# Kernel optimization log

Measured on AMD Instinct MI355X. Metric: run time of the kernel, lower is better.

Reference implementation:

```python
import jax, jax.numpy as jnp
import numpy as np

MARGIN = 0.3
BIG = 1e6  # matches the 1000000.0 additive mask in the torch code


def setup_inputs() -> dict:
    key = jax.random.key(0)
    k1, k2 = jax.random.split(key)
    embeddings = jax.random.normal(k1, (4096, 512), dtype=jnp.float32)
    labels = jax.random.randint(k2, (4096,), 0, 512)
    return {"embeddings": embeddings, "labels": labels}


def reference(embeddings, labels):
    # Pairwise euclidean distances (torch.cdist p=2) via the GEMM identity,
    # clamped before sqrt for numerical safety on the zero diagonal.
    sq = jnp.sum(embeddings * embeddings, axis=1)                      # [N]
    d2 = sq[:, None] + sq[None, :] - 2.0 * (embeddings @ embeddings.T)  # [N, N]
    dist = jnp.sqrt(jnp.maximum(d2, 1e-12))

    pos_mask = labels[None, :] == labels[:, None]   # [N, N] bool
    neg_mask = ~pos_mask

    # Hardest positive per anchor (self-distance 0 is harmless under max).
    hp = jnp.max(dist * pos_mask.astype(dist.dtype), axis=1)           # [N]

    # Semi-hard negatives: hp < d(a, n) < hp + margin, different label.
    semi_hard = (dist > hp[:, None]) & (dist < hp[:, None] + MARGIN) & neg_mask
    has_semi_hard = jnp.sum(semi_hard) > 0

    # Fallback: hardest (farthest) negative; semi-hard branch: closest semi-hard.
    hn_fallback = jnp.max(dist * neg_mask.astype(dist.dtype), axis=1)
    hn_semi = jnp.min(dist + (1.0 - semi_hard.astype(dist.dtype)) * BIG, axis=1)
    hn = jnp.where(has_semi_hard, hn_semi, hn_fallback)                # [N]

    triplet = jax.nn.relu(hp - hn + MARGIN)                            # [N]
    num_valid = jnp.sum((triplet > 0).astype(triplet.dtype))
    loss = jnp.where(num_valid > 0,
                     jnp.sum(triplet) / jnp.maximum(num_valid, 1.0),
                     jnp.mean(triplet))
    return loss
```

## Files before the change

kernel.cpp:

```cpp
#include <hip/hip_runtime.h>
#include <math.h>


constexpr float MARGIN = 0.3f;

typedef _Float16 half8    __attribute__((ext_vector_type(8)));
typedef float    floatx16 __attribute__((ext_vector_type(16)));

#define GLD_LDS16(gp, lp)                                                              \
    __builtin_amdgcn_global_load_lds(                                                  \
        (const __attribute__((address_space(1))) void*)(gp),                           \
        (__attribute__((address_space(3))) void*)(lp), 16, 0, 0)

__global__ __launch_bounds__(256)
void prep_kernel(const float* __restrict__ e, _Float16* __restrict__ pan,
                 float* __restrict__ sq, unsigned int* __restrict__ hp,
                 unsigned int* __restrict__ hn_fall, unsigned int* __restrict__ hn_semi,
                 unsigned int* __restrict__ bars, int N, int D) {
    if (blockIdx.x == 0 && threadIdx.x < 32) bars[threadIdx.x * 32] = 0u;
    const int r0  = blockIdx.x * 32;
    const int p   = r0 >> 7;
    const int rl  = r0 & 127;
    const int r   = threadIdx.x >> 3;
    const int c8  = threadIdx.x & 7;
    const int row = r0 + r;
    const float* er = e + (size_t)row * D;
    float s = 0.f;
    #pragma unroll
    for (int it = 0; it < 8; ++it) {
        const int kw = c8 + it * 8;
        const float4 x0 = *(const float4*)&er[kw * 8];
        const float4 x1 = *(const float4*)&er[kw * 8 + 4];
        const float xv[8] = {x0.x, x0.y, x0.z, x0.w, x1.x, x1.y, x1.z, x1.w};
        half8 hi, lo;
        #pragma unroll
        for (int j = 0; j < 8; ++j) {
            _Float16 h = (_Float16)xv[j];
            hi[j] = h;
            lo[j] = (_Float16)(xv[j] - (float)h);
            s += xv[j] * xv[j];
        }
        *(half8*)&pan[((size_t)(p * 128 + kw) * 128 + rl + r) * 8]      = hi;
        *(half8*)&pan[((size_t)(p * 128 + 64 + kw) * 128 + rl + r) * 8] = lo;
    }
    s += __shfl_down(s, 4, 8);
    s += __shfl_down(s, 2, 8);
    s += __shfl_down(s, 1, 8);
    if (c8 == 0) {
        sq[row]      = s;
        hp[row]      = 0u;
        hn_fall[row] = 0u;
        hn_semi[row] = 0x7f800000u;
    }
}

__global__ __launch_bounds__(512, 4)
void fused_kernel(const _Float16* __restrict__ pan, const int* __restrict__ labels,
                  const float* __restrict__ sq,
                  unsigned int* __restrict__ hp,
                  unsigned int* __restrict__ hn_fall,
                  unsigned int* __restrict__ hn_semi,
                  unsigned int* __restrict__ bars,
                  float* __restrict__ out,
                  int N, int D, unsigned int nrowblocks, unsigned int nblocks) {
    __shared__ __attribute__((aligned(16))) _Float16 S[2][12288];
    __shared__ float sq_r[256], sq_c[128], hp_r[256];
    __shared__ int   lab_r[256], lab_c[128];
    __shared__ int   lastflag;

    const int tid  = threadIdx.x;
    const int lane = tid & 63;
    const int wave = tid >> 6;
    const int wr = (wave >> 1) * 64;
    const int wc = (wave & 1) * 64;
    const int mrow = lane & 31;
    const int half_id = lane >> 5;

    const int j  = blockIdx.x & 7;
    const int i  = blockIdx.x >> 3;
    const int px = (j & 3) * 8 + (i & 7);
    const int py = (j >> 2) * 8 + (i >> 3);
    const int rowBase = py * 256;
    const int colBase = px * 128;

    if (tid < 256) {
        sq_r[tid]  = sq[rowBase + tid];
        lab_r[tid] = labels[rowBase + tid];
    } else if (tid < 384) {
        const int t = tid - 256;
        sq_c[t]  = sq[colBase + t];
        lab_c[t] = labels[colBase + t];
    }

    floatx16 acc[2][2];
    #pragma unroll
    for (int a = 0; a < 2; ++a)
        #pragma unroll
        for (int b = 0; b < 2; ++b)
            #pragma unroll
            for (int r = 0; r < 16; ++r) acc[a][b][r] = 0.f;

    auto stage = [&](int b, int kkv) {
        #pragma unroll
        for (int t = 0; t < 3; ++t) {
            const int s = wave * 3 + t;
            int kcl, p, row0, lofs;
            if (s < 16) {
                const int rq = s & 3;
                kcl  = s >> 2;
                p    = 2 * py + (rq >> 1);
                row0 = (rq & 1) * 64;
                lofs = (kcl * 256 + rq * 64) * 8;
            } else {
                const int u = s - 16;
                kcl  = u >> 1;
                p    = px;
                row0 = (u & 1) * 64;
                lofs = 8192 + (kcl * 128 + row0) * 8;
            }
            const int kc = (kcl < 2) ? (2 * kkv + kcl) : (64 + 2 * kkv + (kcl - 2));
            const _Float16* g = pan + ((size_t)(p * 128 + kc) * 128 + row0 + lane) * 8;
            GLD_LDS16(g, &S[b][lofs]);
        }
    };

    stage(0, 0);

    #pragma unroll 1
    for (int kk = 0; kk < 32; ++kk) {
        const int b = kk & 1;
        __syncthreads();
        if (kk + 1 < 32) stage(b ^ 1, kk + 1);
        const int rA = wr + mrow, cB = wc + mrow;
        const half8 ah0 = *(const half8*)&S[b][(half_id * 256 + rA) * 8];
        const half8 ah1 = *(const half8*)&S[b][(half_id * 256 + rA + 32) * 8];
        const half8 al0 = *(const half8*)&S[b][((2 + half_id) * 256 + rA) * 8];
        const half8 al1 = *(const half8*)&S[b][((2 + half_id) * 256 + rA + 32) * 8];
        const half8 bh0 = *(const half8*)&S[b][8192 + (half_id * 128 + cB) * 8];
        const half8 bh1 = *(const half8*)&S[b][8192 + (half_id * 128 + cB + 32) * 8];
        const half8 bl0 = *(const half8*)&S[b][8192 + ((2 + half_id) * 128 + cB) * 8];
        const half8 bl1 = *(const half8*)&S[b][8192 + ((2 + half_id) * 128 + cB + 32) * 8];
        acc[0][0] = __builtin_amdgcn_mfma_f32_32x32x16_f16(bh0, ah0, acc[0][0], 0, 0, 0);
        acc[0][1] = __builtin_amdgcn_mfma_f32_32x32x16_f16(bh0, ah1, acc[0][1], 0, 0, 0);
        acc[1][0] = __builtin_amdgcn_mfma_f32_32x32x16_f16(bh1, ah0, acc[1][0], 0, 0, 0);
        acc[1][1] = __builtin_amdgcn_mfma_f32_32x32x16_f16(bh1, ah1, acc[1][1], 0, 0, 0);
        acc[0][0] = __builtin_amdgcn_mfma_f32_32x32x16_f16(bl0, ah0, acc[0][0], 0, 0, 0);
        acc[0][1] = __builtin_amdgcn_mfma_f32_32x32x16_f16(bl0, ah1, acc[0][1], 0, 0, 0);
        acc[1][0] = __builtin_amdgcn_mfma_f32_32x32x16_f16(bl1, ah0, acc[1][0], 0, 0, 0);
        acc[1][1] = __builtin_amdgcn_mfma_f32_32x32x16_f16(bl1, ah1, acc[1][1], 0, 0, 0);
        acc[0][0] = __builtin_amdgcn_mfma_f32_32x32x16_f16(bh0, al0, acc[0][0], 0, 0, 0);
        acc[0][1] = __builtin_amdgcn_mfma_f32_32x32x16_f16(bh0, al1, acc[0][1], 0, 0, 0);
        acc[1][0] = __builtin_amdgcn_mfma_f32_32x32x16_f16(bh1, al0, acc[1][0], 0, 0, 0);
        acc[1][1] = __builtin_amdgcn_mfma_f32_32x32x16_f16(bh1, al1, acc[1][1], 0, 0, 0);
    }

    float sqr[2]; int labr[2];
    #pragma unroll
    for (int ai = 0; ai < 2; ++ai) {
        sqr[ai]  = sq_r[wr + ai * 32 + mrow];
        labr[ai] = lab_r[wr + ai * 32 + mrow];
    }

    #pragma unroll
    for (int ai = 0; ai < 2; ++ai) {
        float vp = 0.f, vn = 0.f;
        #pragma unroll
        for (int bj = 0; bj < 2; ++bj) {
            #pragma unroll
            for (int r = 0; r < 16; ++r) {
                const int c = wc + bj * 32 + (r & 3) + 8 * (r >> 2) + 4 * half_id;
                float d = sqrtf(fmaxf(sqr[ai] + sq_c[c] - 2.0f * acc[bj][ai][r], 1e-12f));
                const bool pos = (labr[ai] == lab_c[c]);
                vp = fmaxf(vp, pos ? d : 0.f);
                vn = fmaxf(vn, pos ? 0.f : d);
            }
        }
        vp = fmaxf(vp, __shfl_xor(vp, 32, 64));
        vn = fmaxf(vn, __shfl_xor(vn, 32, 64));
        if (half_id == 0) {
            atomicMax(&hp[rowBase + wr + ai * 32 + mrow],      __float_as_uint(vp));
            atomicMax(&hn_fall[rowBase + wr + ai * 32 + mrow], __float_as_uint(vn));
        }
    }

    __syncthreads();
    unsigned int* ctr = &bars[py * 32];
    if (tid == 0) {
        __threadfence();
        atomicAdd(ctr, 1u);
        while (__hip_atomic_load(ctr, __ATOMIC_ACQUIRE, __HIP_MEMORY_SCOPE_AGENT)
               < nrowblocks)
            __builtin_amdgcn_s_sleep(32);
    }
    __syncthreads();
    if (tid < 256)
        hp_r[tid] = __uint_as_float(__hip_atomic_load(&hp[rowBase + tid],
                                    __ATOMIC_RELAXED, __HIP_MEMORY_SCOPE_AGENT));
    __syncthreads();

    #pragma unroll
    for (int ai = 0; ai < 2; ++ai) {
        const float hpv = hp_r[wr + ai * 32 + mrow];
        float vm = __builtin_inff();
        #pragma unroll
        for (int bj = 0; bj < 2; ++bj) {
            #pragma unroll
            for (int r = 0; r < 16; ++r) {
                const int c = wc + bj * 32 + (r & 3) + 8 * (r >> 2) + 4 * half_id;
                float d = sqrtf(fmaxf(sqr[ai] + sq_c[c] - 2.0f * acc[bj][ai][r], 1e-12f));
                const bool cand = (labr[ai] != lab_c[c]) && (d > hpv);
                vm = fminf(vm, cand ? d : __builtin_inff());
            }
        }
        vm = fminf(vm, __shfl_xor(vm, 32, 64));
        if (half_id == 0)
            atomicMin(&hn_semi[rowBase + wr + ai * 32 + mrow], __float_as_uint(vm));
    }

    __syncthreads();
    if (tid == 0) {
        __threadfence();
        unsigned int old = atomicAdd(&bars[992], 1u);
        lastflag = (old == nblocks - 1) ? 1 : 0;
    }
    __syncthreads();
    if (!lastflag) return;
    if (tid == 0) __threadfence();
    __syncthreads();

    float* FS = (float*)&S[0][0];
    int*   IC = (int*)(FS + 512);
    int*   IA = IC + 512;
    int any = 0;
    for (int r = tid; r < N; r += 512) {
        float h  = __uint_as_float(__hip_atomic_load(&hp[r],      __ATOMIC_RELAXED, __HIP_MEMORY_SCOPE_AGENT));
        float hs = __uint_as_float(__hip_atomic_load(&hn_semi[r], __ATOMIC_RELAXED, __HIP_MEMORY_SCOPE_AGENT));
        any |= (hs < h + MARGIN) ? 1 : 0;
    }
    IA[tid] = any;
    __syncthreads();
    for (int s = 256; s; s >>= 1) {
        if (tid < s) IA[tid] |= IA[tid + s];
        __syncthreads();
    }
    const bool has_semi = IA[0] != 0;
    float sum = 0.f; int valid = 0;
    for (int r = tid; r < N; r += 512) {
        float h  = __uint_as_float(__hip_atomic_load(&hp[r], __ATOMIC_RELAXED, __HIP_MEMORY_SCOPE_AGENT));
        float hn = has_semi
            ? __uint_as_float(__hip_atomic_load(&hn_semi[r], __ATOMIC_RELAXED, __HIP_MEMORY_SCOPE_AGENT))
            : __uint_as_float(__hip_atomic_load(&hn_fall[r], __ATOMIC_RELAXED, __HIP_MEMORY_SCOPE_AGENT));
        float t = fmaxf(h - hn + MARGIN, 0.f);
        if (!(t > 0.f)) t = 0.f;
        sum += t;
        valid += (t > 0.f) ? 1 : 0;
    }
    FS[tid] = sum; IC[tid] = valid;
    __syncthreads();
    for (int s = 256; s; s >>= 1) {
        if (tid < s) { FS[tid] += FS[tid + s]; IC[tid] += IC[tid + s]; }
        __syncthreads();
    }
    if (tid == 0) {
        float total = FS[0]; int v = IC[0];
        out[0] = (v > 0) ? (total / (float)v) : (total / (float)N);
    }
}

extern "C" void kernel_launch(void* const* d_in, const int* in_sizes, int n_in,
                              void* d_out, int out_size, void* d_ws, size_t ws_size,
                              hipStream_t stream) {
    const float* e      = (const float*)d_in[0];
    const int*   labels = (const int*)d_in[1];
    const int N = in_sizes[1];
    const int D = in_sizes[0] / N;
    float* out = (float*)d_out;

    float*        sq      = (float*)d_ws;
    unsigned int* hp      = (unsigned int*)d_ws + N;
    unsigned int* hn_fall = hp + N;
    unsigned int* hn_semi = hn_fall + N;
    unsigned int* bars    = hn_semi + N;

    const size_t small_bytes = ((size_t)(4 * N + 1024) * 4 + 255) & ~(size_t)255;
    _Float16* pan = (_Float16*)((char*)d_ws + small_bytes);

    prep_kernel<<<N / 32, 256, 0, stream>>>(e, pan, sq, hp, hn_fall, hn_semi, bars, N, D);

    const int ntx = N / 128, nty = N / 256;
    fused_kernel<<<ntx * nty, 512, 0, stream>>>(pan, labels, sq, hp, hn_fall, hn_semi,
                                                bars, out, N, D,
                                                (unsigned)ntx, (unsigned)(ntx * nty));
}
```

Before: 139.1 us.

## Exploit distance symmetry: compute only upper-triangle tiles with column-side reductions

Changes the fused kernel to launch only upper-triangular 128x128 tiles of the symmetric distance matrix. Each off-diagonal tile reduces both rows and columns, writing the column maxima and minima through an LDS transpose buffer. The per-row barrier now waits on both the row and the column tile counters. This roughly halves the GEMM and epilogue work, at the cost of extra LDS reductions, more atomics and a more complex spin barrier that requires all blocks to be co-resident. The prep kernel is also re-split to 16 rows per block.

```diff
diff --git a/kernel.cpp b/kernel.cpp
--- a/kernel.cpp
+++ b/kernel.cpp
@@ -17,18 +17,21 @@
                  float* __restrict__ sq, unsigned int* __restrict__ hp,
                  unsigned int* __restrict__ hn_fall, unsigned int* __restrict__ hn_semi,
                  unsigned int* __restrict__ bars, int N, int D) {
-    if (blockIdx.x == 0 && threadIdx.x < 32) bars[threadIdx.x * 32] = 0u;
-    const int r0  = blockIdx.x * 32;
+    if (blockIdx.x == 0) {
+        if (threadIdx.x < 32) bars[threadIdx.x * 32] = 0u;
+        if (threadIdx.x == 32) bars[1023] = 0u;
+    }
+    const int r0  = blockIdx.x * 16;
     const int p   = r0 >> 7;
     const int rl  = r0 & 127;
-    const int r   = threadIdx.x >> 3;
-    const int c8  = threadIdx.x & 7;
+    const int r   = threadIdx.x >> 4;
+    const int c16 = threadIdx.x & 15;
     const int row = r0 + r;
     const float* er = e + (size_t)row * D;
     float s = 0.f;
     #pragma unroll
-    for (int it = 0; it < 8; ++it) {
-        const int kw = c8 + it * 8;
+    for (int it = 0; it < 4; ++it) {
+        const int kw = c16 + it * 16;
         const float4 x0 = *(const float4*)&er[kw * 8];
         const float4 x1 = *(const float4*)&er[kw * 8 + 4];
         const float xv[8] = {x0.x, x0.y, x0.z, x0.w, x1.x, x1.y, x1.z, x1.w};
@@ -43,10 +46,11 @@
         *(half8*)&pan[((size_t)(p * 128 + kw) * 128 + rl + r) * 8]      = hi;
         *(half8*)&pan[((size_t)(p * 128 + 64 + kw) * 128 + rl + r) * 8] = lo;
     }
-    s += __shfl_down(s, 4, 8);
-    s += __shfl_down(s, 2, 8);
-    s += __shfl_down(s, 1, 8);
-    if (c8 == 0) {
+    s += __shfl_down(s, 8, 16);
+    s += __shfl_down(s, 4, 16);
+    s += __shfl_down(s, 2, 16);
+    s += __shfl_down(s, 1, 16);
+    if (c16 == 0) {
         sq[row]      = s;
         hp[row]      = 0u;
         hn_fall[row] = 0u;
@@ -54,7 +58,7 @@
     }
 }
 
-__global__ __launch_bounds__(512, 4)
+__global__ __launch_bounds__(256, 4)
 void fused_kernel(const _Float16* __restrict__ pan, const int* __restrict__ labels,
                   const float* __restrict__ sq,
                   unsigned int* __restrict__ hp,
@@ -62,11 +66,13 @@
                   unsigned int* __restrict__ hn_semi,
                   unsigned int* __restrict__ bars,
                   float* __restrict__ out,
-                  int N, int D, unsigned int nrowblocks, unsigned int nblocks) {
-    __shared__ __attribute__((aligned(16))) _Float16 S[2][12288];
-    __shared__ float sq_r[256], sq_c[128], hp_r[256];
-    __shared__ int   lab_r[256], lab_c[128];
+                  int N, int D, int nt, unsigned int nblocks) {
+    __shared__ __attribute__((aligned(16))) unsigned char SMEM[33024];
+    __shared__ float sq_r[128], sq_c[128], hp_r[128], hp_c[128];
+    __shared__ int   lab_r[128], lab_c[128];
     __shared__ int   lastflag;
+    _Float16* S      = (_Float16*)SMEM;
+    float*    colbuf = (float*)SMEM;
 
     const int tid  = threadIdx.x;
     const int lane = tid & 63;
@@ -76,18 +82,17 @@
     const int mrow = lane & 31;
     const int half_id = lane >> 5;
 
-    const int j  = blockIdx.x & 7;
-    const int i  = blockIdx.x >> 3;
-    const int px = (j & 3) * 8 + (i & 7);
-    const int py = (j >> 2) * 8 + (i >> 3);
-    const int rowBase = py * 256;
-    const int colBase = px * 128;
-
-    if (tid < 256) {
+    int py = 0, rem = blockIdx.x;
+    while (rem >= nt - py) { rem -= nt - py; ++py; }
+    const int px = py + rem;
+    const bool diag = (px == py);
+    const int rowBase = py * 128, colBase = px * 128;
+
+    if (tid < 128) {
         sq_r[tid]  = sq[rowBase + tid];
         lab_r[tid] = labels[rowBase + tid];
-    } else if (tid < 384) {
-        const int t = tid - 256;
+    } else {
+        const int t = tid - 128;
         sq_c[t]  = sq[colBase + t];
         lab_c[t] = labels[colBase + t];
     }
@@ -102,44 +107,34 @@
 
     auto stage = [&](int b, int kkv) {
         #pragma unroll
-        for (int t = 0; t < 3; ++t) {
-            const int s = wave * 3 + t;
-            int kcl, p, row0, lofs;
-            if (s < 16) {
-                const int rq = s & 3;
-                kcl  = s >> 2;
-                p    = 2 * py + (rq >> 1);
-                row0 = (rq & 1) * 64;
-                lofs = (kcl * 256 + rq * 64) * 8;
-            } else {
-                const int u = s - 16;
-                kcl  = u >> 1;
-                p    = px;
-                row0 = (u & 1) * 64;
-                lofs = 8192 + (kcl * 128 + row0) * 8;
-            }
+        for (int t = 0; t < 4; ++t) {
+            const int slab = wave * 4 + t;
+            const int side = slab >> 3;
+            const int u = slab & 7;
+            const int kcl = u >> 1, rh = u & 1;
+            const int pp = side ? px : py;
             const int kc = (kcl < 2) ? (2 * kkv + kcl) : (64 + 2 * kkv + (kcl - 2));
-            const _Float16* g = pan + ((size_t)(p * 128 + kc) * 128 + row0 + lane) * 8;
-            GLD_LDS16(g, &S[b][lofs]);
+            const _Float16* g = pan + ((size_t)(pp * 128 + kc) * 128 + rh * 64 + lane) * 8;
+            GLD_LDS16(g, &S[b * 8192 + side * 4096 + (kcl * 128 + rh * 64) * 8]);
         }
     };
 
     stage(0, 0);
-
     #pragma unroll 1
     for (int kk = 0; kk < 32; ++kk) {
         const int b = kk & 1;
         __syncthreads();
         if (kk + 1 < 32) stage(b ^ 1, kk + 1);
+        const _Float16* Sb = S + b * 8192;
         const int rA = wr + mrow, cB = wc + mrow;
-        const half8 ah0 = *(const half8*)&S[b][(half_id * 256 + rA) * 8];
-        const half8 ah1 = *(const half8*)&S[b][(half_id * 256 + rA + 32) * 8];
-        const half8 al0 = *(const half8*)&S[b][((2 + half_id) * 256 + rA) * 8];
-        const half8 al1 = *(const half8*)&S[b][((2 + half_id) * 256 + rA + 32) * 8];
-        const half8 bh0 = *(const half8*)&S[b][8192 + (half_id * 128 + cB) * 8];
-        const half8 bh1 = *(const half8*)&S[b][8192 + (half_id * 128 + cB + 32) * 8];
-        const half8 bl0 = *(const half8*)&S[b][8192 + ((2 + half_id) * 128 + cB) * 8];
-        const half8 bl1 = *(const half8*)&S[b][8192 + ((2 + half_id) * 128 + cB + 32) * 8];
+        const half8 ah0 = *(const half8*)&Sb[(half_id * 128 + rA) * 8];
+        const half8 ah1 = *(const half8*)&Sb[(half_id * 128 + rA + 32) * 8];
+        const half8 al0 = *(const half8*)&Sb[((2 + half_id) * 128 + rA) * 8];
+        const half8 al1 = *(const half8*)&Sb[((2 + half_id) * 128 + rA + 32) * 8];
+        const half8 bh0 = *(const half8*)&Sb[4096 + (half_id * 128 + cB) * 8];
+        const half8 bh1 = *(const half8*)&Sb[4096 + (half_id * 128 + cB + 32) * 8];
+        const half8 bl0 = *(const half8*)&Sb[4096 + ((2 + half_id) * 128 + cB) * 8];
+        const half8 bl1 = *(const half8*)&Sb[4096 + ((2 + half_id) * 128 + cB + 32) * 8];
         acc[0][0] = __builtin_amdgcn_mfma_f32_32x32x16_f16(bh0, ah0, acc[0][0], 0, 0, 0);
         acc[0][1] = __builtin_amdgcn_mfma_f32_32x32x16_f16(bh0, ah1, acc[0][1], 0, 0, 0);
         acc[1][0] = __builtin_amdgcn_mfma_f32_32x32x16_f16(bh1, ah0, acc[1][0], 0, 0, 0);
@@ -153,6 +148,7 @@
         acc[1][0] = __builtin_amdgcn_mfma_f32_32x32x16_f16(bh1, al0, acc[1][0], 0, 0, 0);
         acc[1][1] = __builtin_amdgcn_mfma_f32_32x32x16_f16(bh1, al1, acc[1][1], 0, 0, 0);
     }
+    __syncthreads();
 
     float sqr[2]; int labr[2];
     #pragma unroll
@@ -160,21 +156,23 @@
         sqr[ai]  = sq_r[wr + ai * 32 + mrow];
         labr[ai] = lab_r[wr + ai * 32 + mrow];
     }
+    auto distf = [&](int bj, int ai, int r, int c) {
+        return sqrtf(fmaxf(sqr[ai] + sq_c[c] - 2.0f * acc[bj][ai][r], 1e-12f));
+    };
 
     #pragma unroll
     for (int ai = 0; ai < 2; ++ai) {
         float vp = 0.f, vn = 0.f;
         #pragma unroll
-        for (int bj = 0; bj < 2; ++bj) {
+        for (int bj = 0; bj < 2; ++bj)
             #pragma unroll
             for (int r = 0; r < 16; ++r) {
                 const int c = wc + bj * 32 + (r & 3) + 8 * (r >> 2) + 4 * half_id;
-                float d = sqrtf(fmaxf(sqr[ai] + sq_c[c] - 2.0f * acc[bj][ai][r], 1e-12f));
+                const float d = distf(bj, ai, r, c);
                 const bool pos = (labr[ai] == lab_c[c]);
                 vp = fmaxf(vp, pos ? d : 0.f);
                 vn = fmaxf(vn, pos ? 0.f : d);
             }
-        }
         vp = fmaxf(vp, __shfl_xor(vp, 32, 64));
         vn = fmaxf(vn, __shfl_xor(vn, 32, 64));
         if (half_id == 0) {
@@ -183,19 +181,54 @@
         }
     }
 
-    __syncthreads();
-    unsigned int* ctr = &bars[py * 32];
+    const int rr = (wave >> 1) * 32 + mrow;
+    if (!diag) {
+        #pragma unroll
+        for (int kind = 0; kind < 2; ++kind) {
+            #pragma unroll
+            for (int bj = 0; bj < 2; ++bj)
+                #pragma unroll
+                for (int r = 0; r < 16; ++r) {
+                    const int c = wc + bj * 32 + (r & 3) + 8 * (r >> 2) + 4 * half_id;
+                    const float d0 = distf(bj, 0, r, c);
+                    const float d1 = distf(bj, 1, r, c);
+                    const bool p0 = (labr[0] == lab_c[c]), p1 = (labr[1] == lab_c[c]);
+                    float v;
+                    if (kind == 0) v = fmaxf(p0 ? d0 : 0.f, p1 ? d1 : 0.f);
+                    else           v = fmaxf(p0 ? 0.f : d0, p1 ? 0.f : d1);
+                    colbuf[rr * 129 + c] = v;
+                }
+            __syncthreads();
+            if (tid < 128) {
+                float v = 0.f;
+                #pragma unroll 4
+                for (int q = 0; q < 64; ++q) v = fmaxf(v, colbuf[q * 129 + tid]);
+                if (kind == 0) atomicMax(&hp[colBase + tid],      __float_as_uint(v));
+                else           atomicMax(&hn_fall[colBase + tid], __float_as_uint(v));
+            }
+            __syncthreads();
+        }
+    }
+
+    __syncthreads();
     if (tid == 0) {
         __threadfence();
-        atomicAdd(ctr, 1u);
-        while (__hip_atomic_load(ctr, __ATOMIC_ACQUIRE, __HIP_MEMORY_SCOPE_AGENT)
-               < nrowblocks)
-            __builtin_amdgcn_s_sleep(32);
-    }
-    __syncthreads();
-    if (tid < 256)
+        atomicAdd(&bars[py * 32], 1u);
+        if (!diag) atomicAdd(&bars[px * 32], 1u);
+        while (__hip_atomic_load(&bars[py * 32], __ATOMIC_ACQUIRE, __HIP_MEMORY_SCOPE_AGENT)
+               < (unsigned)nt) __builtin_amdgcn_s_sleep(32);
+        while (__hip_atomic_load(&bars[px * 32], __ATOMIC_ACQUIRE, __HIP_MEMORY_SCOPE_AGENT)
+               < (unsigned)nt) __builtin_amdgcn_s_sleep(32);
+    }
+    __syncthreads();
+    if (tid < 128)
         hp_r[tid] = __uint_as_float(__hip_atomic_load(&hp[rowBase + tid],
                                     __ATOMIC_RELAXED, __HIP_MEMORY_SCOPE_AGENT));
+    else {
+        const int t = tid - 128;
+        hp_c[t] = __uint_as_float(__hip_atomic_load(&hp[colBase + t],
+                                  __ATOMIC_RELAXED, __HIP_MEMORY_SCOPE_AGENT));
+    }
     __syncthreads();
 
     #pragma unroll
@@ -203,24 +236,46 @@
         const float hpv = hp_r[wr + ai * 32 + mrow];
         float vm = __builtin_inff();
         #pragma unroll
-        for (int bj = 0; bj < 2; ++bj) {
+        for (int bj = 0; bj < 2; ++bj)
             #pragma unroll
             for (int r = 0; r < 16; ++r) {
                 const int c = wc + bj * 32 + (r & 3) + 8 * (r >> 2) + 4 * half_id;
-                float d = sqrtf(fmaxf(sqr[ai] + sq_c[c] - 2.0f * acc[bj][ai][r], 1e-12f));
+                const float d = distf(bj, ai, r, c);
                 const bool cand = (labr[ai] != lab_c[c]) && (d > hpv);
                 vm = fminf(vm, cand ? d : __builtin_inff());
             }
-        }
         vm = fminf(vm, __shfl_xor(vm, 32, 64));
         if (half_id == 0)
             atomicMin(&hn_semi[rowBase + wr + ai * 32 + mrow], __float_as_uint(vm));
     }
 
+    if (!diag) {
+        #pragma unroll
+        for (int bj = 0; bj < 2; ++bj)
+            #pragma unroll
+            for (int r = 0; r < 16; ++r) {
+                const int c = wc + bj * 32 + (r & 3) + 8 * (r >> 2) + 4 * half_id;
+                const float hpv = hp_c[c];
+                const float d0 = distf(bj, 0, r, c);
+                const float d1 = distf(bj, 1, r, c);
+                const bool c0 = (labr[0] != lab_c[c]) && (d0 > hpv);
+                const bool c1 = (labr[1] != lab_c[c]) && (d1 > hpv);
+                colbuf[rr * 129 + c] = fminf(c0 ? d0 : __builtin_inff(),
+                                             c1 ? d1 : __builtin_inff());
+            }
+        __syncthreads();
+        if (tid < 128) {
+            float v = __builtin_inff();
+            #pragma unroll 4
+            for (int q = 0; q < 64; ++q) v = fminf(v, colbuf[q * 129 + tid]);
+            atomicMin(&hn_semi[colBase + tid], __float_as_uint(v));
+        }
+    }
+
     __syncthreads();
     if (tid == 0) {
         __threadfence();
-        unsigned int old = atomicAdd(&bars[992], 1u);
+        unsigned int old = atomicAdd(&bars[1023], 1u);
         lastflag = (old == nblocks - 1) ? 1 : 0;
     }
     __syncthreads();
@@ -228,24 +283,24 @@
     if (tid == 0) __threadfence();
     __syncthreads();
 
-    float* FS = (float*)&S[0][0];
-    int*   IC = (int*)(FS + 512);
-    int*   IA = IC + 512;
+    float* FS = (float*)SMEM;
+    int*   IC = (int*)(FS + 256);
+    int*   IA = IC + 256;
     int any = 0;
-    for (int r = tid; r < N; r += 512) {
+    for (int r = tid; r < N; r += 256) {
         float h  = __uint_as_float(__hip_atomic_load(&hp[r],      __ATOMIC_RELAXED, __HIP_MEMORY_SCOPE_AGENT));
         float hs = __uint_as_float(__hip_atomic_load(&hn_semi[r], __ATOMIC_RELAXED, __HIP_MEMORY_SCOPE_AGENT));
         any |= (hs < h + MARGIN) ? 1 : 0;
     }
     IA[tid] = any;
     __syncthreads();
-    for (int s = 256; s; s >>= 1) {
+    for (int s = 128; s; s >>= 1) {
         if (tid < s) IA[tid] |= IA[tid + s];
         __syncthreads();
     }
     const bool has_semi = IA[0] != 0;
     float sum = 0.f; int valid = 0;
-    for (int r = tid; r < N; r += 512) {
+    for (int r = tid; r < N; r += 256) {
         float h  = __uint_as_float(__hip_atomic_load(&hp[r], __ATOMIC_RELAXED, __HIP_MEMORY_SCOPE_AGENT));
         float hn = has_semi
             ? __uint_as_float(__hip_atomic_load(&hn_semi[r], __ATOMIC_RELAXED, __HIP_MEMORY_SCOPE_AGENT))
@@ -257,7 +312,7 @@
     }
     FS[tid] = sum; IC[tid] = valid;
     __syncthreads();
-    for (int s = 256; s; s >>= 1) {
+    for (int s = 128; s; s >>= 1) {
         if (tid < s) { FS[tid] += FS[tid + s]; IC[tid] += IC[tid + s]; }
         __syncthreads();
     }
@@ -285,10 +340,10 @@
     const size_t small_bytes = ((size_t)(4 * N + 1024) * 4 + 255) & ~(size_t)255;
     _Float16* pan = (_Float16*)((char*)d_ws + small_bytes);
 
-    prep_kernel<<<N / 32, 256, 0, stream>>>(e, pan, sq, hp, hn_fall, hn_semi, bars, N, D);
-
-    const int ntx = N / 128, nty = N / 256;
-    fused_kernel<<<ntx * nty, 512, 0, stream>>>(pan, labels, sq, hp, hn_fall, hn_semi,
-                                                bars, out, N, D,
-                                                (unsigned)ntx, (unsigned)(ntx * nty));
+    prep_kernel<<<N / 16, 256, 0, stream>>>(e, pan, sq, hp, hn_fall, hn_semi, bars, N, D);
+
+    const int nt = N / 128;
+    const int nblocks = nt * (nt + 1) / 2;
+    fused_kernel<<<nblocks, 256, 0, stream>>>(pan, labels, sq, hp, hn_fall, hn_semi,
+                                              bars, out, N, D, nt, (unsigned)nblocks);
 }
```

Result: slower. 151.6 us (+9.0%).

## Convert fp32 to split fp16 inside GEMM loop and defer sqrt to finalize

Applied to the files above, without the earlier changes.

Drops the separate prepacked fp16 hi/lo panel buffer. The fused kernel now loads fp32 embeddings into registers, splits them into hi/lo halves and writes them to LDS, with register prefetch of the next k-slice. It also keeps squared distances through the max/min reductions and applies sqrt only in the final reduction, removing per-element sqrt from the epilogue. This trades the panel write and read round trip for redundant conversion work in every tile and ordinary global loads in place of the direct global-to-LDS loads.

```diff
diff --git a/kernel.cpp b/kernel.cpp
--- a/kernel.cpp
+++ b/kernel.cpp
@@ -7,59 +7,39 @@
 typedef _Float16 half8    __attribute__((ext_vector_type(8)));
 typedef float    floatx16 __attribute__((ext_vector_type(16)));
 
-#define GLD_LDS16(gp, lp)                                                              \
-    __builtin_amdgcn_global_load_lds(                                                  \
-        (const __attribute__((address_space(1))) void*)(gp),                           \
-        (__attribute__((address_space(3))) void*)(lp), 16, 0, 0)
-
 __global__ __launch_bounds__(256)
-void prep_kernel(const float* __restrict__ e, _Float16* __restrict__ pan,
-                 float* __restrict__ sq, unsigned int* __restrict__ hp,
-                 unsigned int* __restrict__ hn_fall, unsigned int* __restrict__ hn_semi,
-                 unsigned int* __restrict__ bars, int N, int D) {
+void sq_init_kernel(const float* __restrict__ e, float* __restrict__ sq,
+                    unsigned int* __restrict__ hp2, unsigned int* __restrict__ hnf2,
+                    unsigned int* __restrict__ hns2, unsigned int* __restrict__ bars,
+                    int N, int D) {
     if (blockIdx.x == 0 && threadIdx.x < 32) bars[threadIdx.x * 32] = 0u;
-    const int r0  = blockIdx.x * 32;
-    const int p   = r0 >> 7;
-    const int rl  = r0 & 127;
-    const int r   = threadIdx.x >> 3;
-    const int c8  = threadIdx.x & 7;
-    const int row = r0 + r;
+    const int row  = blockIdx.x * 4 + (threadIdx.x >> 6);
+    const int lane = threadIdx.x & 63;
+    if (row >= N) return;
     const float* er = e + (size_t)row * D;
     float s = 0.f;
-    #pragma unroll
-    for (int it = 0; it < 8; ++it) {
-        const int kw = c8 + it * 8;
-        const float4 x0 = *(const float4*)&er[kw * 8];
-        const float4 x1 = *(const float4*)&er[kw * 8 + 4];
-        const float xv[8] = {x0.x, x0.y, x0.z, x0.w, x1.x, x1.y, x1.z, x1.w};
-        half8 hi, lo;
-        #pragma unroll
-        for (int j = 0; j < 8; ++j) {
-            _Float16 h = (_Float16)xv[j];
-            hi[j] = h;
-            lo[j] = (_Float16)(xv[j] - (float)h);
-            s += xv[j] * xv[j];
-        }
-        *(half8*)&pan[((size_t)(p * 128 + kw) * 128 + rl + r) * 8]      = hi;
-        *(half8*)&pan[((size_t)(p * 128 + 64 + kw) * 128 + rl + r) * 8] = lo;
-    }
-    s += __shfl_down(s, 4, 8);
-    s += __shfl_down(s, 2, 8);
-    s += __shfl_down(s, 1, 8);
-    if (c8 == 0) {
-        sq[row]      = s;
-        hp[row]      = 0u;
-        hn_fall[row] = 0u;
-        hn_semi[row] = 0x7f800000u;
+    for (int k0 = lane * 8; k0 < D; k0 += 512) {
+        const float4 x0 = *(const float4*)&er[k0];
+        const float4 x1 = *(const float4*)&er[k0 + 4];
+        s += x0.x*x0.x + x0.y*x0.y + x0.z*x0.z + x0.w*x0.w
+           + x1.x*x1.x + x1.y*x1.y + x1.z*x1.z + x1.w*x1.w;
+    }
+    #pragma unroll
+    for (int off = 32; off; off >>= 1) s += __shfl_down(s, off, 64);
+    if (lane == 0) {
+        sq[row]   = s;
+        hp2[row]  = 0u;
+        hnf2[row] = 0u;
+        hns2[row] = 0x7f800000u;
     }
 }
 
 __global__ __launch_bounds__(512, 4)
-void fused_kernel(const _Float16* __restrict__ pan, const int* __restrict__ labels,
+void fused_kernel(const float* __restrict__ e, const int* __restrict__ labels,
                   const float* __restrict__ sq,
-                  unsigned int* __restrict__ hp,
-                  unsigned int* __restrict__ hn_fall,
-                  unsigned int* __restrict__ hn_semi,
+                  unsigned int* __restrict__ hp2,
+                  unsigned int* __restrict__ hnf2,
+                  unsigned int* __restrict__ hns2,
                   unsigned int* __restrict__ bars,
                   float* __restrict__ out,
                   int N, int D, unsigned int nrowblocks, unsigned int nblocks) {
@@ -100,37 +80,53 @@
             #pragma unroll
             for (int r = 0; r < 16; ++r) acc[a][b][r] = 0.f;
 
-    auto stage = [&](int b, int kkv) {
-        #pragma unroll
-        for (int t = 0; t < 3; ++t) {
-            const int s = wave * 3 + t;
-            int kcl, p, row0, lofs;
-            if (s < 16) {
-                const int rq = s & 3;
-                kcl  = s >> 2;
-                p    = 2 * py + (rq >> 1);
-                row0 = (rq & 1) * 64;
-                lofs = (kcl * 256 + rq * 64) * 8;
-            } else {
-                const int u = s - 16;
-                kcl  = u >> 1;
-                p    = px;
-                row0 = (u & 1) * 64;
-                lofs = 8192 + (kcl * 128 + row0) * 8;
-            }
-            const int kc = (kcl < 2) ? (2 * kkv + kcl) : (64 + 2 * kkv + (kcl - 2));
-            const _Float16* g = pan + ((size_t)(p * 128 + kc) * 128 + row0 + lane) * 8;
-            GLD_LDS16(g, &S[b][lofs]);
+    const int srow = tid >> 1, sch = tid & 1;
+    float4 ra0, ra1, rb0, rb1;
+    auto loadRegs = [&](int kkv) {
+        const float* ga = &e[(size_t)(rowBase + srow) * D + kkv * 16 + sch * 8];
+        ra0 = *(const float4*)ga;
+        ra1 = *(const float4*)(ga + 4);
+        if (tid < 256) {
+            const float* gb = &e[(size_t)(colBase + srow) * D + kkv * 16 + sch * 8];
+            rb0 = *(const float4*)gb;
+            rb1 = *(const float4*)(gb + 4);
         }
     };
-
-    stage(0, 0);
+    auto cvtWrite = [&](int b) {
+        {
+            const float xv[8] = {ra0.x, ra0.y, ra0.z, ra0.w, ra1.x, ra1.y, ra1.z, ra1.w};
+            half8 hi, lo;
+            #pragma unroll
+            for (int q = 0; q < 8; ++q) {
+                _Float16 h = (_Float16)xv[q];
+                hi[q] = h;
+                lo[q] = (_Float16)(xv[q] - (float)h);
+            }
+            *(half8*)&S[b][(sch * 256 + srow) * 8]       = hi;
+            *(half8*)&S[b][((2 + sch) * 256 + srow) * 8] = lo;
+        }
+        if (tid < 256) {
+            const float xv[8] = {rb0.x, rb0.y, rb0.z, rb0.w, rb1.x, rb1.y, rb1.z, rb1.w};
+            half8 hi, lo;
+            #pragma unroll
+            for (int q = 0; q < 8; ++q) {
+                _Float16 h = (_Float16)xv[q];
+                hi[q] = h;
+                lo[q] = (_Float16)(xv[q] - (float)h);
+            }
+            *(half8*)&S[b][8192 + (sch * 128 + srow) * 8]       = hi;
+            *(half8*)&S[b][8192 + ((2 + sch) * 128 + srow) * 8] = lo;
+        }
+    };
+
+    loadRegs(0);
 
     #pragma unroll 1
     for (int kk = 0; kk < 32; ++kk) {
         const int b = kk & 1;
+        cvtWrite(b);
         __syncthreads();
-        if (kk + 1 < 32) stage(b ^ 1, kk + 1);
+        if (kk + 1 < 32) loadRegs(kk + 1);
         const int rA = wr + mrow, cB = wc + mrow;
         const half8 ah0 = *(const half8*)&S[b][(half_id * 256 + rA) * 8];
         const half8 ah1 = *(const half8*)&S[b][(half_id * 256 + rA + 32) * 8];
@@ -169,17 +165,17 @@
             #pragma unroll
             for (int r = 0; r < 16; ++r) {
                 const int c = wc + bj * 32 + (r & 3) + 8 * (r >> 2) + 4 * half_id;
-                float d = sqrtf(fmaxf(sqr[ai] + sq_c[c] - 2.0f * acc[bj][ai][r], 1e-12f));
+                const float d2 = fmaxf(sqr[ai] + sq_c[c] - 2.0f * acc[bj][ai][r], 1e-12f);
                 const bool pos = (labr[ai] == lab_c[c]);
-                vp = fmaxf(vp, pos ? d : 0.f);
-                vn = fmaxf(vn, pos ? 0.f : d);
+                vp = fmaxf(vp, pos ? d2 : 0.f);
+                vn = fmaxf(vn, pos ? 0.f : d2);
             }
         }
         vp = fmaxf(vp, __shfl_xor(vp, 32, 64));
         vn = fmaxf(vn, __shfl_xor(vn, 32, 64));
         if (half_id == 0) {
-            atomicMax(&hp[rowBase + wr + ai * 32 + mrow],      __float_as_uint(vp));
-            atomicMax(&hn_fall[rowBase + wr + ai * 32 + mrow], __float_as_uint(vn));
+            atomicMax(&hp2[rowBase + wr + ai * 32 + mrow],  __float_as_uint(vp));
+            atomicMax(&hnf2[rowBase + wr + ai * 32 + mrow], __float_as_uint(vn));
         }
     }
 
@@ -194,27 +190,27 @@
     }
     __syncthreads();
     if (tid < 256)
-        hp_r[tid] = __uint_as_float(__hip_atomic_load(&hp[rowBase + tid],
+        hp_r[tid] = __uint_as_float(__hip_atomic_load(&hp2[rowBase + tid],
                                     __ATOMIC_RELAXED, __HIP_MEMORY_SCOPE_AGENT));
     __syncthreads();
 
     #pragma unroll
     for (int ai = 0; ai < 2; ++ai) {
-        const float hpv = hp_r[wr + ai * 32 + mrow];
+        const float hpv2 = hp_r[wr + ai * 32 + mrow];
         float vm = __builtin_inff();
         #pragma unroll
         for (int bj = 0; bj < 2; ++bj) {
             #pragma unroll
             for (int r = 0; r < 16; ++r) {
                 const int c = wc + bj * 32 + (r & 3) + 8 * (r >> 2) + 4 * half_id;
-                float d = sqrtf(fmaxf(sqr[ai] + sq_c[c] - 2.0f * acc[bj][ai][r], 1e-12f));
-                const bool cand = (labr[ai] != lab_c[c]) && (d > hpv);
-                vm = fminf(vm, cand ? d : __builtin_inff());
+                const float d2 = fmaxf(sqr[ai] + sq_c[c] - 2.0f * acc[bj][ai][r], 1e-12f);
+                const bool cand = (labr[ai] != lab_c[c]) && (d2 > hpv2);
+                vm = fminf(vm, cand ? d2 : __builtin_inff());
             }
         }
         vm = fminf(vm, __shfl_xor(vm, 32, 64));
         if (half_id == 0)
-            atomicMin(&hn_semi[rowBase + wr + ai * 32 + mrow], __float_as_uint(vm));
+            atomicMin(&hns2[rowBase + wr + ai * 32 + mrow], __float_as_uint(vm));
     }
 
     __syncthreads();
@@ -233,8 +229,8 @@
     int*   IA = IC + 512;
     int any = 0;
     for (int r = tid; r < N; r += 512) {
-        float h  = __uint_as_float(__hip_atomic_load(&hp[r],      __ATOMIC_RELAXED, __HIP_MEMORY_SCOPE_AGENT));
-        float hs = __uint_as_float(__hip_atomic_load(&hn_semi[r], __ATOMIC_RELAXED, __HIP_MEMORY_SCOPE_AGENT));
+        float h  = sqrtf(__uint_as_float(__hip_atomic_load(&hp2[r],  __ATOMIC_RELAXED, __HIP_MEMORY_SCOPE_AGENT)));
+        float hs = sqrtf(__uint_as_float(__hip_atomic_load(&hns2[r], __ATOMIC_RELAXED, __HIP_MEMORY_SCOPE_AGENT)));
         any |= (hs < h + MARGIN) ? 1 : 0;
     }
     IA[tid] = any;
@@ -246,10 +242,10 @@
     const bool has_semi = IA[0] != 0;
     float sum = 0.f; int valid = 0;
     for (int r = tid; r < N; r += 512) {
-        float h  = __uint_as_float(__hip_atomic_load(&hp[r], __ATOMIC_RELAXED, __HIP_MEMORY_SCOPE_AGENT));
+        float h  = sqrtf(__uint_as_float(__hip_atomic_load(&hp2[r], __ATOMIC_RELAXED, __HIP_MEMORY_SCOPE_AGENT)));
         float hn = has_semi
-            ? __uint_as_float(__hip_atomic_load(&hn_semi[r], __ATOMIC_RELAXED, __HIP_MEMORY_SCOPE_AGENT))
-            : __uint_as_float(__hip_atomic_load(&hn_fall[r], __ATOMIC_RELAXED, __HIP_MEMORY_SCOPE_AGENT));
+            ? sqrtf(__uint_as_float(__hip_atomic_load(&hns2[r], __ATOMIC_RELAXED, __HIP_MEMORY_SCOPE_AGENT)))
+            : sqrtf(__uint_as_float(__hip_atomic_load(&hnf2[r], __ATOMIC_RELAXED, __HIP_MEMORY_SCOPE_AGENT)));
         float t = fmaxf(h - hn + MARGIN, 0.f);
         if (!(t > 0.f)) t = 0.f;
         sum += t;
@@ -276,19 +272,16 @@
     const int D = in_sizes[0] / N;
     float* out = (float*)d_out;
 
-    float*        sq      = (float*)d_ws;
-    unsigned int* hp      = (unsigned int*)d_ws + N;
-    unsigned int* hn_fall = hp + N;
-    unsigned int* hn_semi = hn_fall + N;
-    unsigned int* bars    = hn_semi + N;
-
-    const size_t small_bytes = ((size_t)(4 * N + 1024) * 4 + 255) & ~(size_t)255;
-    _Float16* pan = (_Float16*)((char*)d_ws + small_bytes);
-
-    prep_kernel<<<N / 32, 256, 0, stream>>>(e, pan, sq, hp, hn_fall, hn_semi, bars, N, D);
+    float*        sq   = (float*)d_ws;
+    unsigned int* hp2  = (unsigned int*)d_ws + N;
+    unsigned int* hnf2 = hp2 + N;
+    unsigned int* hns2 = hnf2 + N;
+    unsigned int* bars = hns2 + N;
+
+    sq_init_kernel<<<N / 4, 256, 0, stream>>>(e, sq, hp2, hnf2, hns2, bars, N, D);
 
     const int ntx = N / 128, nty = N / 256;
-    fused_kernel<<<ntx * nty, 512, 0, stream>>>(pan, labels, sq, hp, hn_fall, hn_semi,
+    fused_kernel<<<ntx * nty, 512, 0, stream>>>(e, labels, sq, hp2, hnf2, hns2,
                                                 bars, out, N, D,
                                                 (unsigned)ntx, (unsigned)(ntx * nty));
 }
```

New measurement: 146.4 us. +5.3%, slower.

## Load A operand fragments directly from global memory, stage only B in LDS

Applied to the files above, without the earlier changes.

The A-tile (row) fragments are now read straight from global memory into registers each k-step instead of going through the shared-memory double buffer. Only the B (column) tile is still staged in LDS, which shrinks the shared buffer from 48KB to 16KB and removes A's LDS write/read traffic. Each pair of waves sharing rows now fetches the same A data from global/L2 separately. The global loads issue before the barrier with no explicit prefetch, so their latency may sit on the critical path.

```diff
diff --git a/kernel.cpp b/kernel.cpp
--- a/kernel.cpp
+++ b/kernel.cpp
@@ -63,7 +63,7 @@
                   unsigned int* __restrict__ bars,
                   float* __restrict__ out,
                   int N, int D, unsigned int nrowblocks, unsigned int nblocks) {
-    __shared__ __attribute__((aligned(16))) _Float16 S[2][12288];
+    __shared__ __attribute__((aligned(16))) _Float16 S[2][4096];
     __shared__ float sq_r[256], sq_c[128], hp_r[256];
     __shared__ int   lab_r[256], lab_c[128];
     __shared__ int   lastflag;
@@ -100,46 +100,34 @@
             #pragma unroll
             for (int r = 0; r < 16; ++r) acc[a][b][r] = 0.f;
 
-    auto stage = [&](int b, int kkv) {
-        #pragma unroll
-        for (int t = 0; t < 3; ++t) {
-            const int s = wave * 3 + t;
-            int kcl, p, row0, lofs;
-            if (s < 16) {
-                const int rq = s & 3;
-                kcl  = s >> 2;
-                p    = 2 * py + (rq >> 1);
-                row0 = (rq & 1) * 64;
-                lofs = (kcl * 256 + rq * 64) * 8;
-            } else {
-                const int u = s - 16;
-                kcl  = u >> 1;
-                p    = px;
-                row0 = (u & 1) * 64;
-                lofs = 8192 + (kcl * 128 + row0) * 8;
-            }
-            const int kc = (kcl < 2) ? (2 * kkv + kcl) : (64 + 2 * kkv + (kcl - 2));
-            const _Float16* g = pan + ((size_t)(p * 128 + kc) * 128 + row0 + lane) * 8;
-            GLD_LDS16(g, &S[b][lofs]);
-        }
+    const int pA = 2 * py + (wr >> 7);
+    const size_t aBase = ((size_t)(pA * 128 + half_id) * 128 + (wr & 127) + mrow) * 8;
+    const size_t loOff = (size_t)64 * 128 * 8;
+
+    auto stageB = [&](int b, int kkv) {
+        const int kcl = wave >> 1, rh = wave & 1;
+        const int kc = (kcl < 2) ? (2 * kkv + kcl) : (64 + 2 * kkv + (kcl - 2));
+        const _Float16* g = pan + ((size_t)(px * 128 + kc) * 128 + rh * 64 + lane) * 8;
+        GLD_LDS16(g, &S[b][(kcl * 128 + rh * 64) * 8]);
     };
 
-    stage(0, 0);
+    stageB(0, 0);
 
     #pragma unroll 1
     for (int kk = 0; kk < 32; ++kk) {
         const int b = kk & 1;
+        const _Float16* ga = pan + aBase + (size_t)kk * 2048;
+        const half8 ah0 = *(const half8*)(ga);
+        const half8 ah1 = *(const half8*)(ga + 256);
+        const half8 al0 = *(const half8*)(ga + loOff);
+        const half8 al1 = *(const half8*)(ga + loOff + 256);
         __syncthreads();
-        if (kk + 1 < 32) stage(b ^ 1, kk + 1);
-        const int rA = wr + mrow, cB = wc + mrow;
-        const half8 ah0 = *(const half8*)&S[b][(half_id * 256 + rA) * 8];
-        const half8 ah1 = *(const half8*)&S[b][(half_id * 256 + rA + 32) * 8];
-        const half8 al0 = *(const half8*)&S[b][((2 + half_id) * 256 + rA) * 8];
-        const half8 al1 = *(const half8*)&S[b][((2 + half_id) * 256 + rA + 32) * 8];
-        const half8 bh0 = *(const half8*)&S[b][8192 + (half_id * 128 + cB) * 8];
-        const half8 bh1 = *(const half8*)&S[b][8192 + (half_id * 128 + cB + 32) * 8];
-        const half8 bl0 = *(const half8*)&S[b][8192 + ((2 + half_id) * 128 + cB) * 8];
-        const half8 bl1 = *(const half8*)&S[b][8192 + ((2 + half_id) * 128 + cB + 32) * 8];
+        if (kk + 1 < 32) stageB(b ^ 1, kk + 1);
+        const int cB = wc + mrow;
+        const half8 bh0 = *(const half8*)&S[b][(half_id * 128 + cB) * 8];
+        const half8 bh1 = *(const half8*)&S[b][(half_id * 128 + cB + 32) * 8];
+        const half8 bl0 = *(const half8*)&S[b][((2 + half_id) * 128 + cB) * 8];
+        const half8 bl1 = *(const half8*)&S[b][((2 + half_id) * 128 + cB + 32) * 8];
         acc[0][0] = __builtin_amdgcn_mfma_f32_32x32x16_f16(bh0, ah0, acc[0][0], 0, 0, 0);
         acc[0][1] = __builtin_amdgcn_mfma_f32_32x32x16_f16(bh0, ah1, acc[0][1], 0, 0, 0);
         acc[1][0] = __builtin_amdgcn_mfma_f32_32x32x16_f16(bh1, ah0, acc[1][0], 0, 0, 0);
```

Result: slower. 151.0 us (+8.6%).
